# Kernel optimization log

Measured on AMD Instinct MI355X. Metric: run time of the kernel, lower is better.

The kernel has to match this reference:

```python
import jax, jax.numpy as jnp
import numpy as np

B, S, H = 2, 2048, 4096
N_HEADS, N_KV_HEADS, HEAD_DIM = 32, 8, 128
WINDOW = 1024
ROPE_THETA = 10000.0


def rotate_half(x):
    x1, x2 = jnp.split(x, 2, axis=-1)
    return jnp.concatenate((-x2, x1), axis=-1)


def rope_cache(seq_len, head_dim, theta):
    inv_freq = 1.0 / (theta ** (jnp.arange(0, head_dim, 2, dtype=jnp.float32) / head_dim))
    t = jnp.arange(seq_len, dtype=jnp.float32)
    freqs = jnp.outer(t, inv_freq)                      # [S, hd/2]
    emb = jnp.concatenate((freqs, freqs), axis=-1)      # [S, hd]
    return jnp.cos(emb), jnp.sin(emb)


def setup_inputs() -> dict:
    key = jax.random.key(0)
    k0, k1, k2, k3, k4 = jax.random.split(key, 5)
    sc_in = 1.0 / np.sqrt(H)
    return {
        "hidden_states": jax.random.normal(k0, (B, S, H), dtype=jnp.float32),
        "Wq": jax.random.normal(k1, (N_HEADS * HEAD_DIM, H), dtype=jnp.float32) * sc_in,
        "Wk": jax.random.normal(k2, (N_KV_HEADS * HEAD_DIM, H), dtype=jnp.float32) * sc_in,
        "Wv": jax.random.normal(k3, (N_KV_HEADS * HEAD_DIM, H), dtype=jnp.float32) * sc_in,
        "Wo": jax.random.normal(k4, (H, N_HEADS * HEAD_DIM), dtype=jnp.float32) * sc_in,
        "position_ids": jnp.tile(jnp.arange(S, dtype=jnp.int64 if jax.config.jax_enable_x64 else jnp.int32), (B, 1)),
    }


def reference(hidden_states, Wq, Wk, Wv, Wo, position_ids):
    b, s, h = hidden_states.shape
    n_rep = N_HEADS // N_KV_HEADS

    # projections (Linear with no bias: x @ W.T)
    q = (hidden_states @ Wq.T).reshape(b, s, N_HEADS, HEAD_DIM).transpose(0, 2, 1, 3)
    k = (hidden_states @ Wk.T).reshape(b, s, N_KV_HEADS, HEAD_DIM).transpose(0, 2, 1, 3)
    v = (hidden_states @ Wv.T).reshape(b, s, N_KV_HEADS, HEAD_DIM).transpose(0, 2, 1, 3)

    # RoPE
    cos_c, sin_c = rope_cache(s, HEAD_DIM, ROPE_THETA)
    cos = cos_c[position_ids][:, None]  # [b,1,s,hd]
    sin = sin_c[position_ids][:, None]
    q = q * cos + rotate_half(q) * sin
    k = k * cos + rotate_half(k) * sin

    # GQA repeat_kv
    k = jnp.repeat(k, n_rep, axis=1)  # [b, n_heads, s, hd]
    v = jnp.repeat(v, n_rep, axis=1)

    # sliding-window causal attention
    scores = jnp.einsum('bhqd,bhkd->bhqk', q, k) / jnp.sqrt(jnp.asarray(HEAD_DIM, q.dtype))
    i = jnp.arange(s)[:, None]
    j = jnp.arange(s)[None, :]
    allowed = (j <= i) & ((i - j) < WINDOW)  # causal + sliding window
    scores = jnp.where(allowed, scores, jnp.finfo(scores.dtype).min)
    attn = jax.nn.softmax(scores.astype(jnp.float32), axis=-1).astype(q.dtype)

    out = jnp.einsum('bhqk,bhkd->bhqd', attn, v)  # [b,h,s,hd]
    out = out.transpose(0, 2, 1, 3).reshape(b, s, N_HEADS * HEAD_DIM)
    return out @ Wo.T
```

## Files before the change

### kernel.cpp

```cpp
#include <hip/hip_runtime.h>
#include <hip/hip_bf16.h>
#include <cmath>

typedef unsigned short u16;
typedef __attribute__((ext_vector_type(8))) short bf16x8;
typedef __attribute__((ext_vector_type(4))) float f32x4;
typedef __attribute__((ext_vector_type(16))) float f32x16;
typedef __attribute__((ext_vector_type(2))) int i32x2;
typedef __attribute__((ext_vector_type(4))) unsigned int u32x4;

#define B_    2
#define S_    2048
#define H_    4096
#define NH_   32
#define NKV_  8
#define HD_   128
#define WIN_  1024

__device__ __forceinline__ u16 f2b(float f) {
  union { float f; unsigned u; } v; v.f = f;
  unsigned r = v.u + 0x7fffu + ((v.u >> 16) & 1u);
  return (u16)(r >> 16);
}
__device__ __forceinline__ float b2f(u16 h) {
  union { unsigned u; float f; } v; v.u = ((unsigned)h) << 16;
  return v.f;
}

__device__ __forceinline__ void storeC(float* p, float v) { *p = v; }
__device__ __forceinline__ void storeC(u16* p, float v)   { *p = f2b(v); }

__device__ __forceinline__ void gl2lds(const u16* g, u16* l) {
  __builtin_amdgcn_global_load_lds(
      (const __attribute__((address_space(1))) unsigned int*)(g),
      (__attribute__((address_space(3))) unsigned int*)(l), 16, 0, 0);
}

__device__ __forceinline__ i32x2 plswap(int a, int b) {
  return __builtin_amdgcn_permlane32_swap(a, b, false, false);
}
__device__ __forceinline__ unsigned pkbf16(float lo, float hi) {
  unsigned r;
  asm("v_cvt_pk_bf16_f32 %0, %1, %2" : "=v"(r) : "v"(lo), "v"(hi));
  return r;
}

__global__ __launch_bounds__(256) void cvt_bf16(const float* __restrict__ s,
                                                u16* __restrict__ d, int n4) {
  int i = blockIdx.x * 256 + threadIdx.x;
  if (i < n4) {
    float4 v = ((const float4*)s)[i];
    ushort4 o;
    o.x = f2b(v.x); o.y = f2b(v.y); o.z = f2b(v.z); o.w = f2b(v.w);
    ((ushort4*)d)[i] = o;
  }
}

template <int BM, typename OutT>
__global__ __launch_bounds__(256) void gemm_bt(const u16* __restrict__ A,
                                               const u16* __restrict__ W,
                                               OutT* __restrict__ C,
                                               int M, int N, int K) {
  __shared__ u16 As[BM * 32];
  __shared__ u16 Bs[128 * 32];
  const int t = threadIdx.x;
  const int lane = t & 63, wave = t >> 6;
  const int quad = lane >> 4, l16 = lane & 15;
  const int wm = wave >> 1, wn = wave & 1;
  constexpr int WM = BM / 2;
  constexpr int MI = WM / 16;
  const size_t m0 = (size_t)blockIdx.y * BM, n0 = (size_t)blockIdx.x * 128;

  f32x4 acc[MI][4] = {};
  const int srow = lane >> 2, skc = lane & 3;

  for (int k0 = 0; k0 < K; k0 += 32) {
    __syncthreads();
#pragma unroll
    for (int i = 0; i < BM / 64; i++) {
      int row = wave * (BM / 4) + i * 16 + srow;
      gl2lds(A + (m0 + row) * K + k0 + skc * 8, &As[row * 32 + skc * 8]);
    }
#pragma unroll
    for (int i = 0; i < 2; i++) {
      int row = wave * 32 + i * 16 + srow;
      gl2lds(W + (n0 + row) * K + k0 + skc * 8, &Bs[row * 32 + skc * 8]);
    }
    __syncthreads();
    bf16x8 af[MI], bfr[4];
#pragma unroll
    for (int i = 0; i < MI; i++)
      af[i] = *(const bf16x8*)(&As[(wm * WM + i * 16 + l16) * 32 + quad * 8]);
#pragma unroll
    for (int i = 0; i < 4; i++)
      bfr[i] = *(const bf16x8*)(&Bs[(wn * 64 + i * 16 + l16) * 32 + quad * 8]);
#pragma unroll
    for (int mi = 0; mi < MI; mi++)
#pragma unroll
      for (int nj = 0; nj < 4; nj++)
        acc[mi][nj] = __builtin_amdgcn_mfma_f32_16x16x32_bf16(
            af[mi], bfr[nj], acc[mi][nj], 0, 0, 0);
  }

#pragma unroll
  for (int mi = 0; mi < MI; mi++) {
    size_t rbase = m0 + wm * WM + mi * 16 + quad * 4;
#pragma unroll
    for (int nj = 0; nj < 4; nj++) {
      size_t col = n0 + wn * 64 + nj * 16 + l16;
#pragma unroll
      for (int e = 0; e < 4; e++)
        storeC(&C[(rbase + e) * N + col], acc[mi][nj][e]);
    }
  }
}

template <typename OutT>
__global__ __launch_bounds__(512, 1) void gemm256(const u16* __restrict__ A,
                                                  const u16* __restrict__ W,
                                                  OutT* __restrict__ C,
                                                  int M, int N, int K) {
  __shared__ __align__(16) u16 smem[65536];
  const int t = threadIdx.x;
  const int lane = t & 63, wave = t >> 6;
  const int quad = lane >> 4, l16 = lane & 15;
  const int wm = wave >> 2, wn = wave & 3;

  const int wg = blockIdx.x;
  const int swz = (wg & 7) * ((int)gridDim.x >> 3) + (wg >> 3);
  const int nbn = N >> 8;
  const size_t m0 = (size_t)(swz / nbn) * 256, n0 = (size_t)(swz % nbn) * 256;

  f32x4 acc[8][4] = {};

  const int srow0 = wave * 32;
  const int sr = lane >> 3, sj = lane & 7;

  auto stage = [&](int bsel, int kt) {
    u16* ab = smem + bsel * 16384;
    u16* bb = smem + 32768 + bsel * 16384;
#pragma unroll
    for (int ii = 0; ii < 4; ii++) {
      int row = srow0 + ii * 8 + sr;
      int gb = (sj ^ (row & 7)) * 8;
      gl2lds(A + (m0 + row) * K + kt + gb, ab + (srow0 + ii * 8) * 64 + lane * 8);
      gl2lds(W + (n0 + row) * K + kt + gb, bb + (srow0 + ii * 8) * 64 + lane * 8);
    }
  };

  stage(0, 0);
  __syncthreads();
  int buf = 0;
  for (int kt = 0; kt < K; kt += 64) {
    if (kt + 64 < K) stage(buf ^ 1, kt + 64);
    const u16* ab = smem + buf * 16384;
    const u16* bb = smem + 32768 + buf * 16384;

    bf16x8 bfr[4][2];
#pragma unroll
    for (int nj = 0; nj < 4; nj++) {
      int row = wn * 64 + nj * 16 + l16;
#pragma unroll
      for (int ks = 0; ks < 2; ks++)
        bfr[nj][ks] = *(const bf16x8*)(bb + row * 64 + (((ks * 4 + quad) ^ (row & 7)) * 8));
    }
#pragma unroll
    for (int p = 0; p < 4; p++) {
      bf16x8 af[2][2];
#pragma unroll
      for (int mm = 0; mm < 2; mm++) {
        int row = wm * 128 + (p * 2 + mm) * 16 + l16;
#pragma unroll
        for (int ks = 0; ks < 2; ks++)
          af[mm][ks] = *(const bf16x8*)(ab + row * 64 + (((ks * 4 + quad) ^ (row & 7)) * 8));
      }
      __builtin_amdgcn_s_setprio(1);
#pragma unroll
      for (int mm = 0; mm < 2; mm++)
#pragma unroll
        for (int nj = 0; nj < 4; nj++)
#pragma unroll
          for (int ks = 0; ks < 2; ks++)
            acc[p * 2 + mm][nj] = __builtin_amdgcn_mfma_f32_16x16x32_bf16(
                af[mm][ks], bfr[nj][ks], acc[p * 2 + mm][nj], 0, 0, 0);
      __builtin_amdgcn_s_setprio(0);
    }
    __syncthreads();
    buf ^= 1;
  }

#pragma unroll
  for (int mi = 0; mi < 8; mi++) {
    size_t rbase = m0 + wm * 128 + mi * 16 + quad * 4;
#pragma unroll
    for (int nj = 0; nj < 4; nj++) {
      size_t col = n0 + wn * 64 + nj * 16 + l16;
#pragma unroll
      for (int e = 0; e < 4; e++)
        storeC(&C[(rbase + e) * N + col], acc[mi][nj][e]);
    }
  }
}

__global__ __launch_bounds__(256) void rope_k(u16* __restrict__ X,
                                              const int* __restrict__ pos,
                                              int log2nh) {
  int idx = blockIdx.x * 256 + threadIdx.x;
  int i = idx & 63;
  int bsh = idx >> 6;
  int h = bsh & ((1 << log2nh) - 1);
  int bs = bsh >> log2nh;
  int p = pos[bs];
  float inv = exp2f(-(float)i * (13.287712379549449f / 64.0f));
  float ang = (float)p * inv;
  float sn, c;
  sincosf(ang, &sn, &c);
  size_t base = ((((size_t)bs) << log2nh) + h) * HD_;
  float x1 = b2f(X[base + i]), x2 = b2f(X[base + i + 64]);
  X[base + i]      = f2b(x1 * c - x2 * sn);
  X[base + i + 64] = f2b(x2 * c + x1 * sn);
}

__global__ __launch_bounds__(256) void transpose_v(const u16* __restrict__ V,
                                                   u16* __restrict__ Vt) {
  __shared__ u16 tile[64][72];
  int s0 = blockIdx.x * 64, d0 = blockIdx.y * 64, bh = blockIdx.z;
  int b = bh >> 3, hk = bh & 7;
  int t = threadIdx.x;
  int r = t >> 3, c = t & 7;
#pragma unroll
  for (int i = 0; i < 2; i++) {
    int row = r + i * 32;
    uint4 v = *(const uint4*)(V + (((size_t)(b * S_ + s0 + row)) * NKV_ + hk) * HD_ + d0 + c * 8);
    *(uint4*)(&tile[row][c * 8]) = v;
  }
  __syncthreads();
#pragma unroll
  for (int i = 0; i < 2; i++) {
    int d = r + i * 32;
    u16 tmp[8];
#pragma unroll
    for (int j = 0; j < 8; j++) tmp[j] = tile[c * 8 + j][d];
    *(uint4*)(Vt + ((size_t)bh * HD_ + d0 + d) * S_ + s0 + c * 8) = *(uint4*)tmp;
  }
}

__global__ __launch_bounds__(256, 2) void attn_k(const u16* __restrict__ Q,
                                                 const u16* __restrict__ K,
                                                 const u16* __restrict__ Vt,
                                                 u16* __restrict__ O) {
  __shared__ __align__(16) u16 smem[32768];
  const int t = threadIdx.x, wave = t >> 6, lane = t & 63;
  const int cq = lane & 31, hi = lane >> 5;
  const int q0 = blockIdx.x * 128, h = blockIdx.y, b = blockIdx.z;
  const int hk = h >> 2;
  const int qw = q0 + wave * 32;
  const int q = qw + cq;
  const float SCL2 = 0.08838834764831845f * 1.4426950408889634f;

  bf16x8 qf[8];
  {
    const u16* qp = Q + ((size_t)(b * S_ + q) * NH_ + h) * HD_ + hi * 8;
#pragma unroll
    for (int c = 0; c < 8; c++) qf[c] = *(const bf16x8*)(qp + c * 16);
  }

  f32x16 oacc[4] = {};
  float m_i = -1e30f, l_i = 0.0f;

  const int rK = wave * 16 + (lane >> 4), jKl = lane & 15;
  const int rV = wave * 32 + (lane >> 3), jVl = lane & 7;
  const size_t kbase0 = (size_t)b * S_ * (NKV_ * HD_) + (size_t)hk * HD_;
  const size_t vbase0 = (size_t)(b * NKV_ + hk) * HD_ * S_;

  auto stage = [&](int bsel, int kt) {
    u16* kd = smem + bsel * 8192 + wave * 2048 + lane * 8;
    u16* vd = smem + 16384 + bsel * 8192 + wave * 2048 + lane * 8;
#pragma unroll
    for (int ii = 0; ii < 4; ii++) {
      int row = rK + 4 * ii;
      gl2lds(K + kbase0 + (size_t)(kt + row) * (NKV_ * HD_) + (jKl ^ (row & 7)) * 8,
             kd + ii * 512);
    }
#pragma unroll
    for (int ii = 0; ii < 4; ii++) {
      int row = rV + 8 * ii;
      gl2lds(Vt + vbase0 + (size_t)row * S_ + kt + (jVl ^ (row & 7)) * 8,
             vd + ii * 512);
    }
  };

  int lo = q0 - (WIN_ - 1); if (lo < 0) lo = 0;
  const int lo_t = lo & ~63;
  const int kt_max = q0 + 64;

  stage(0, lo_t);
  __syncthreads();
  int buf = 0;
  for (int kt = lo_t; kt <= kt_max; kt += 64) {
    if (kt + 64 <= kt_max) stage(buf ^ 1, kt + 64);
    if (kt <= qw + 31 && kt + 63 >= qw - (WIN_ - 1)) {
      const u16* ks = smem + buf * 8192;
      const u16* vs = smem + 16384 + buf * 8192;
      const int rx = cq & 7;
      f32x16 cs0 = {}, cs1 = {};
      __builtin_amdgcn_s_setprio(1);
#pragma unroll
      for (int c = 0; c < 8; c++) {
        const int blk = 2 * c + hi;
        bf16x8 a0 = *(const bf16x8*)(ks + cq * 128 + ((blk ^ rx) * 8));
        bf16x8 a1 = *(const bf16x8*)(ks + (32 + cq) * 128 + ((blk ^ rx) * 8));
        cs0 = __builtin_amdgcn_mfma_f32_32x32x16_bf16(a0, qf[c], cs0, 0, 0, 0);
        cs1 = __builtin_amdgcn_mfma_f32_32x32x16_bf16(a1, qf[c], cs1, 0, 0, 0);
      }
      __builtin_amdgcn_s_setprio(0);

      float sv[32];
      const bool full = (kt >= qw - 992) && (kt + 63 <= qw);
      if (full) {
#pragma unroll
        for (int r = 0; r < 16; r++) {
          sv[r] = cs0[r] * SCL2;
          sv[16 + r] = cs1[r] * SCL2;
        }
      } else {
#pragma unroll
        for (int g = 0; g < 2; g++)
#pragma unroll
          for (int r = 0; r < 16; r++) {
            int kk = kt + g * 32 + (r & 3) + 8 * (r >> 2) + 4 * hi;
            float s = (g ? cs1[r] : cs0[r]) * SCL2;
            sv[g * 16 + r] = (kk <= q && q - kk < WIN_) ? s : -1e30f;
          }
      }

      float m4[4] = {sv[0], sv[1], sv[2], sv[3]};
#pragma unroll
      for (int i = 4; i < 32; i++) m4[i & 3] = fmaxf(m4[i & 3], sv[i]);
      float mx = fmaxf(fmaxf(m4[0], m4[1]), fmaxf(m4[2], m4[3]));
      {
        i32x2 r2 = plswap(__float_as_int(mx), __float_as_int(mx));
        mx = fmaxf(__int_as_float(r2.x), __int_as_float(r2.y));
      }
      if (__any(mx > m_i + 8.0f)) {
        float mn = fmaxf(m_i, mx);
        float al = exp2f(m_i - mn);
        m_i = mn; l_i *= al;
#pragma unroll
        for (int dg = 0; dg < 4; dg++)
#pragma unroll
          for (int e = 0; e < 16; e++) oacc[dg][e] *= al;
      }
      float p[32], a4[4] = {0.f, 0.f, 0.f, 0.f};
#pragma unroll
      for (int i = 0; i < 32; i++) {
        p[i] = exp2f(sv[i] - m_i);
        a4[i & 3] += p[i];
      }
      float rs = (a4[0] + a4[1]) + (a4[2] + a4[3]);
      {
        i32x2 r2 = plswap(__float_as_int(rs), __float_as_int(rs));
        rs = __int_as_float(r2.x) + __int_as_float(r2.y);
      }
      l_i += rs;

      bf16x8 pb[4];
#pragma unroll
      for (int cc = 0; cc < 4; cc++) {
        const int bse = cc * 8;
        unsigned x0 = pkbf16(p[bse + 0], p[bse + 1]);
        unsigned y0 = pkbf16(p[bse + 4], p[bse + 5]);
        unsigned x1 = pkbf16(p[bse + 2], p[bse + 3]);
        unsigned y1 = pkbf16(p[bse + 6], p[bse + 7]);
        i32x2 w02 = plswap((int)x0, (int)y0);
        i32x2 w13 = plswap((int)x1, (int)y1);
        u32x4 wv;
        wv.x = (unsigned)w02.x; wv.y = (unsigned)w13.x;
        wv.z = (unsigned)w02.y; wv.w = (unsigned)w13.y;
        pb[cc] = __builtin_bit_cast(bf16x8, wv);
      }

      __builtin_amdgcn_s_setprio(1);
#pragma unroll
      for (int dg = 0; dg < 4; dg++) {
        const int rr = dg * 32 + cq;
#pragma unroll
        for (int cc = 0; cc < 4; cc++) {
          bf16x8 va = *(const bf16x8*)(vs + rr * 64 + (((2 * cc + hi) ^ (rr & 7)) * 8));
          oacc[dg] = __builtin_amdgcn_mfma_f32_32x32x16_bf16(va, pb[cc], oacc[dg], 0, 0, 0);
        }
      }
      __builtin_amdgcn_s_setprio(0);
    }
    __syncthreads();
    buf ^= 1;
  }

  const float inv = 1.0f / l_i;
  u16* os = smem + wave * 4352;
#pragma unroll
  for (int dg = 0; dg < 4; dg++)
#pragma unroll
    for (int e = 0; e < 16; e += 2) {
      int d = dg * 32 + (e & 3) + 8 * (e >> 2) + 4 * hi;
      unsigned pk2 = (unsigned)f2b(oacc[dg][e] * inv) |
                     ((unsigned)f2b(oacc[dg][e + 1] * inv) << 16);
      *(unsigned*)(os + cq * 136 + d) = pk2;
    }
  asm volatile("s_waitcnt lgkmcnt(0)" ::: "memory");
  __builtin_amdgcn_sched_barrier(0);
#pragma unroll
  for (int ps = 0; ps < 8; ps++) {
    int row = (lane >> 4) + ps * 4, j = lane & 15;
    uint4 vv = *(const uint4*)(os + row * 136 + j * 8);
    *(uint4*)(O + ((size_t)(b * S_ + q0 + wave * 32 + row) * NH_ + h) * HD_ + j * 8) = vv;
  }
}

extern "C" void kernel_launch(void* const* d_in, const int* in_sizes, int n_in,
                              void* d_out, int out_size, void* d_ws, size_t ws_size,
                              hipStream_t stream) {
  const float* x  = (const float*)d_in[0];
  const float* Wq = (const float*)d_in[1];
  const float* Wk = (const float*)d_in[2];
  const float* Wv = (const float*)d_in[3];
  const float* Wo = (const float*)d_in[4];
  const int*  pos = (const int*)d_in[5];
  float* out = (float*)d_out;

  const size_t BS = (size_t)B_ * S_;
  const size_t MB = 1024 * 1024;
  char* p = (char*)d_ws;
  u16* xb  = (u16*)(p);
  u16* W32 = (u16*)(p + 32 * MB);
  u16* W8  = (u16*)(p + 64 * MB);
  u16* Qb  = (u16*)(p + 72 * MB);
  u16* Kb  = (u16*)(p + 104 * MB);
  u16* Vb  = (u16*)(p + 112 * MB);
  u16* WoB = xb;
  u16* Ob  = W32;
  u16* Vt  = W8;

  auto cvt = [&](const float* src, u16* dst, size_t n) {
    int n4 = (int)(n / 4);
    cvt_bf16<<<dim3((n4 + 255) / 256), dim3(256), 0, stream>>>(src, dst, n4);
  };

  cvt(x, xb, BS * H_);
  cvt(Wq, W32, (size_t)H_ * H_);
  gemm256<u16><<<dim3(256), dim3(512), 0, stream>>>(xb, W32, Qb, (int)BS, H_, H_);
  cvt(Wk, W8, (size_t)NKV_ * HD_ * H_);
  gemm_bt<64, u16><<<dim3(NKV_ * HD_ / 128, BS / 64), dim3(256), 0, stream>>>(
      xb, W8, Kb, (int)BS, NKV_ * HD_, H_);
  cvt(Wv, W8, (size_t)NKV_ * HD_ * H_);
  gemm_bt<64, u16><<<dim3(NKV_ * HD_ / 128, BS / 64), dim3(256), 0, stream>>>(
      xb, W8, Vb, (int)BS, NKV_ * HD_, H_);

  rope_k<<<dim3((int)(BS * NH_ * 64 / 256)), dim3(256), 0, stream>>>(Qb, pos, 5);
  rope_k<<<dim3((int)(BS * NKV_ * 64 / 256)), dim3(256), 0, stream>>>(Kb, pos, 3);

  transpose_v<<<dim3(S_ / 64, HD_ / 64, B_ * NKV_), dim3(256), 0, stream>>>(Vb, Vt);

  attn_k<<<dim3(S_ / 128, NH_, B_), dim3(256), 0, stream>>>(Qb, Kb, Vt, Ob);

  cvt(Wo, WoB, (size_t)H_ * H_);
  gemm256<float><<<dim3(256), dim3(512), 0, stream>>>(Ob, WoB, out, (int)BS, H_, H_);
}
```

Measured before the change: 766.5 us.

## Deepen GEMM pipeline to four K=32 LDS stages with explicit vmcnt waits

The 256x256 GEMM's LDS staging changes from two buffers of K=64 to four ring slots of K=32. Loads are issued two iterations ahead, and each slot is waited on with s_waitcnt vmcnt counts instead of a full __syncthreads drain. This aims to keep more global-to-LDS loads in flight and overlap them with MFMA work. The cost is more barriers per unit of K and half the MFMA work per iteration. Correctness also depends on the hand-computed vmcnt counts and on reusing a slot only after the second barrier.

```diff
diff --git a/kernel.cpp b/kernel.cpp
--- a/kernel.cpp
+++ b/kernel.cpp
@@ -134,59 +134,63 @@
   f32x4 acc[8][4] = {};
 
   const int srow0 = wave * 32;
-  const int sr = lane >> 3, sj = lane & 7;
-
-  auto stage = [&](int bsel, int kt) {
-    u16* ab = smem + bsel * 16384;
-    u16* bb = smem + 32768 + bsel * 16384;
-#pragma unroll
-    for (int ii = 0; ii < 4; ii++) {
-      int row = srow0 + ii * 8 + sr;
-      int gb = (sj ^ (row & 7)) * 8;
-      gl2lds(A + (m0 + row) * K + kt + gb, ab + (srow0 + ii * 8) * 64 + lane * 8);
-      gl2lds(W + (n0 + row) * K + kt + gb, bb + (srow0 + ii * 8) * 64 + lane * 8);
+  const int sr = lane >> 2, sj = lane & 3;
+
+  auto stage = [&](int slot, int kt) {
+    u16* sb = smem + slot * 16384;
+#pragma unroll
+    for (int half = 0; half < 2; half++) {
+      int row = srow0 + half * 16 + sr;
+      int gb = (sj ^ (row & 3)) * 8;
+      gl2lds(A + (m0 + row) * K + kt + gb,
+             sb + (srow0 + half * 16) * 32 + lane * 8);
+      gl2lds(W + (n0 + row) * K + kt + gb,
+             sb + 8192 + (srow0 + half * 16) * 32 + lane * 8);
     }
   };
 
+  const int nk = K >> 5;
   stage(0, 0);
-  __syncthreads();
-  int buf = 0;
-  for (int kt = 0; kt < K; kt += 64) {
-    if (kt + 64 < K) stage(buf ^ 1, kt + 64);
-    const u16* ab = smem + buf * 16384;
-    const u16* bb = smem + 32768 + buf * 16384;
-
-    bf16x8 bfr[4][2];
+  stage(1, 32);
+  for (int i = 0; i < nk; i++) {
+    if (i + 2 < nk) stage((i + 2) & 3, (i + 2) << 5);
+    if (i + 2 < nk) {
+      asm volatile("s_waitcnt vmcnt(8)" ::: "memory");
+    } else if (i + 1 < nk) {
+      asm volatile("s_waitcnt vmcnt(4)" ::: "memory");
+    } else {
+      asm volatile("s_waitcnt vmcnt(0)" ::: "memory");
+    }
+    __builtin_amdgcn_sched_barrier(0);
+    __builtin_amdgcn_s_barrier();
+
+    const u16* ab = smem + (i & 3) * 16384;
+    const u16* bb = ab + 8192;
+    bf16x8 bfr[4];
 #pragma unroll
     for (int nj = 0; nj < 4; nj++) {
       int row = wn * 64 + nj * 16 + l16;
-#pragma unroll
-      for (int ks = 0; ks < 2; ks++)
-        bfr[nj][ks] = *(const bf16x8*)(bb + row * 64 + (((ks * 4 + quad) ^ (row & 7)) * 8));
+      bfr[nj] = *(const bf16x8*)(bb + row * 32 + ((quad ^ (row & 3)) * 8));
     }
 #pragma unroll
     for (int p = 0; p < 4; p++) {
-      bf16x8 af[2][2];
+      bf16x8 af[2];
 #pragma unroll
       for (int mm = 0; mm < 2; mm++) {
         int row = wm * 128 + (p * 2 + mm) * 16 + l16;
-#pragma unroll
-        for (int ks = 0; ks < 2; ks++)
-          af[mm][ks] = *(const bf16x8*)(ab + row * 64 + (((ks * 4 + quad) ^ (row & 7)) * 8));
+        af[mm] = *(const bf16x8*)(ab + row * 32 + ((quad ^ (row & 3)) * 8));
       }
       __builtin_amdgcn_s_setprio(1);
 #pragma unroll
       for (int mm = 0; mm < 2; mm++)
 #pragma unroll
         for (int nj = 0; nj < 4; nj++)
-#pragma unroll
-          for (int ks = 0; ks < 2; ks++)
-            acc[p * 2 + mm][nj] = __builtin_amdgcn_mfma_f32_16x16x32_bf16(
-                af[mm][ks], bfr[nj][ks], acc[p * 2 + mm][nj], 0, 0, 0);
+          acc[p * 2 + mm][nj] = __builtin_amdgcn_mfma_f32_16x16x32_bf16(
+              af[mm], bfr[nj], acc[p * 2 + mm][nj], 0, 0, 0);
       __builtin_amdgcn_s_setprio(0);
     }
-    __syncthreads();
-    buf ^= 1;
+    __builtin_amdgcn_sched_barrier(0);
+    __builtin_amdgcn_s_barrier();
   }
 
 #pragma unroll
```

Result: no change. 780.5 us (+1.8%).
